# Performance work log

Measured on AMD Instinct MI355X. Metric: run time of the kernel, lower is better.

The kernel has to match this reference:

```python
import jax, jax.numpy as jnp
import numpy as np

B, T = 4, 2048
H, NH, NKV, HD = 2048, 16, 4, 128
THETA = 10000.0
SCALE = HD ** -0.5


def setup_inputs() -> dict:
    key = jax.random.key(0)
    ks = jax.random.split(key, 9)
    s = lambda n: 1.0 / np.sqrt(n)
    return {
        "hidden_states": jax.random.normal(ks[0], (B, T, H), jnp.float32),
        "positions": jnp.tile(jnp.arange(T, dtype=jnp.int32)[None, :], (B, 1)),
        "wq": jax.random.normal(ks[1], (H, NH * HD), jnp.float32) * s(H),
        "bq": jax.random.normal(ks[2], (NH * HD,), jnp.float32) * 0.01,
        "wk": jax.random.normal(ks[3], (H, NKV * HD), jnp.float32) * s(H),
        "bk": jax.random.normal(ks[4], (NKV * HD,), jnp.float32) * 0.01,
        "wv": jax.random.normal(ks[5], (H, NKV * HD), jnp.float32) * s(H),
        "bv": jax.random.normal(ks[6], (NKV * HD,), jnp.float32) * 0.01,
        "wo": jax.random.normal(ks[7], (NH * HD, H), jnp.float32) * s(NH * HD),
    }


def _rope(x, pos):
    # Neox-style RoPE over full head_dim. x: [B,T,n,HD], pos: [B,T]
    half = HD // 2
    inv_freq = 1.0 / (THETA ** (jnp.arange(half, dtype=jnp.float32) / half))
    freqs = pos.astype(jnp.float32)[..., None] * inv_freq  # [B,T,half]
    cos = jnp.cos(freqs)[:, :, None, :]
    sin = jnp.sin(freqs)[:, :, None, :]
    x1, x2 = x[..., :half], x[..., half:]
    return jnp.concatenate([x1 * cos - x2 * sin, x2 * cos + x1 * sin], axis=-1)


def reference(hidden_states, wq, bq, wk, bk, wv, bv, wo, positions):
    q = (hidden_states @ wq + bq).reshape(B, T, NH, HD)
    k = (hidden_states @ wk + bk).reshape(B, T, NKV, HD)
    v = (hidden_states @ wv + bv).reshape(B, T, NKV, HD)
    q = _rope(q, positions)
    k = _rope(k, positions)
    # GQA: repeat kv heads to match query heads
    rep = NH // NKV
    k = jnp.repeat(k, rep, axis=2)
    v = jnp.repeat(v, rep, axis=2)
    q = q.transpose(0, 2, 1, 3)  # [B,NH,T,HD]
    k = k.transpose(0, 2, 1, 3)
    v = v.transpose(0, 2, 1, 3)
    scores = jnp.einsum('bhqd,bhkd->bhqk', q, k) * SCALE
    causal = jnp.tril(jnp.ones((T, T), dtype=jnp.bool_))
    scores = jnp.where(causal[None, None, :, :], scores, -jnp.inf)
    w = jax.nn.softmax(scores, axis=-1).astype(v.dtype)
    o = jnp.einsum('bhqk,bhkd->bhqd', w, v)
    o = o.transpose(0, 2, 1, 3).reshape(B, T, NH * HD)
    return o @ wo
```

## Files before the change

kernel.cpp:

```cpp
#include <hip/hip_runtime.h>
#include <hip/hip_bf16.h>

#define TSEQ 2048
#define BATCH 4
#define NH 16
#define NKV 4
#define HD 128
#define NQKV 3072
#define SCALE_ 0.08838834764831845f

typedef __bf16 bf16x8 __attribute__((ext_vector_type(8)));
typedef float f32x4 __attribute__((ext_vector_type(4)));

__device__ __forceinline__ unsigned short f2bf(float f) {
    union { float f; unsigned u; } v; v.f = f;
    unsigned r = v.u + 0x7fffu + ((v.u >> 16) & 1u);
    return (unsigned short)(r >> 16);
}
__device__ __forceinline__ float bf2f(unsigned short b) {
    union { unsigned u; float f; } v; v.u = ((unsigned)b) << 16; return v.f;
}

__global__ __launch_bounds__(256) void xconv(const float* __restrict__ in,
                                             unsigned short* __restrict__ out) {
    const size_t i = (size_t)blockIdx.x * 256 + threadIdx.x;
    const float4 v = ((const float4*)in)[i];
    union { unsigned short u[4]; int2 p; } o;
    o.u[0] = f2bf(v.x); o.u[1] = f2bf(v.y); o.u[2] = f2bf(v.z); o.u[3] = f2bf(v.w);
    ((int2*)out)[i] = o.p;
}

__global__ __launch_bounds__(256) void wtrans_kernel(const float* __restrict__ in,
                                                     unsigned short* __restrict__ out,
                                                     int inN, int K) {
    __shared__ unsigned short l[64][65];
    const int n0 = blockIdx.x * 64, k0 = blockIdx.y * 64;
    const int tid = threadIdx.x;
    const int r = tid >> 2, c0 = (tid & 3) * 16;
#pragma unroll
    for (int i = 0; i < 16; i += 4) {
        float4 v = *(const float4*)&in[(size_t)(k0 + r) * inN + n0 + c0 + i];
        l[c0 + i + 0][r] = f2bf(v.x);
        l[c0 + i + 1][r] = f2bf(v.y);
        l[c0 + i + 2][r] = f2bf(v.z);
        l[c0 + i + 3][r] = f2bf(v.w);
    }
    __syncthreads();
    unsigned short tmp[16];
#pragma unroll
    for (int i = 0; i < 16; ++i) tmp[i] = l[r][c0 + i];
    *(int4*)&out[(size_t)(n0 + r) * K + k0 + c0] = *(int4*)&tmp[0];
    *(int4*)&out[(size_t)(n0 + r) * K + k0 + c0 + 8] = *(int4*)&tmp[8];
}

__global__ __launch_bounds__(256) void bias_concat(const float* __restrict__ bq,
                                                   const float* __restrict__ bk,
                                                   const float* __restrict__ bv,
                                                   float* __restrict__ out) {
    int i = blockIdx.x * 256 + threadIdx.x;
    out[i] = (i < 2048) ? bq[i] : ((i < 2560) ? bk[i - 2048] : bv[i - 2560]);
}

template <bool BIAS, bool OUTBF16>
__global__ __launch_bounds__(512) void gemm256(const unsigned short* __restrict__ A,
                                               const unsigned short* __restrict__ Bt,
                                               const float* __restrict__ bias,
                                               void* __restrict__ Cout,
                                               int M, int N, int K, int mtiles) {
    __shared__ unsigned short lA[2][256 * 64];
    __shared__ unsigned short lB[2][256 * 64];
    const int tid = threadIdx.x, lane = tid & 63, wid = tid >> 6;
    const int wr = wid >> 2, wc = wid & 3;
    const int g = lane >> 4, lr = lane & 15;
    const int nwg = gridDim.x;
    const int q = nwg >> 3;
    const int wg = (blockIdx.x & 7) * q + (blockIdx.x >> 3);
    const int bm = (wg % mtiles) * 256, bn = (wg / mtiles) * 256;

    f32x4 acc[8][4];
#pragma unroll
    for (int m = 0; m < 8; ++m)
#pragma unroll
        for (int n = 0; n < 4; ++n) acc[m][n] = f32x4{0.f, 0.f, 0.f, 0.f};

    auto stage = [&](int buf, int k0) {
#pragma unroll
        for (int c = 0; c < 4; ++c) {
            const int soff = (c * 512 + tid) * 16;
            const int row = soff >> 7;
            const int chunk = ((soff >> 4) & 7) ^ (row & 7);
            const unsigned lbase = (unsigned)(c * 512 + wid * 64) * 16;
            __builtin_amdgcn_global_load_lds(
                (const __attribute__((address_space(1))) unsigned int*)
                    (A + (size_t)(bm + row) * K + k0 + chunk * 8),
                (__attribute__((address_space(3))) unsigned int*)((char*)lA[buf] + lbase),
                16, 0, 0);
            __builtin_amdgcn_global_load_lds(
                (const __attribute__((address_space(1))) unsigned int*)
                    (Bt + (size_t)(bn + row) * K + k0 + chunk * 8),
                (__attribute__((address_space(3))) unsigned int*)((char*)lB[buf] + lbase),
                16, 0, 0);
        }
    };

    stage(0, 0);
    const int NT = K >> 6;
    for (int t = 0; t < NT; ++t) {
        const int buf = t & 1;
        if (t + 1 < NT) stage(buf ^ 1, (t + 1) << 6);
        __builtin_amdgcn_sched_barrier(0);
        if (t + 1 < NT) {
            asm volatile("s_waitcnt vmcnt(8)" ::: "memory");
        } else {
            asm volatile("s_waitcnt vmcnt(0)" ::: "memory");
        }
        __builtin_amdgcn_s_barrier();
        __builtin_amdgcn_sched_barrier(0);
        const char* pa = (const char*)lA[buf];
        const char* pb = (const char*)lB[buf];
#pragma unroll
        for (int kk = 0; kk < 2; ++kk) {
            bf16x8 bfr[4];
#pragma unroll
            for (int n = 0; n < 4; ++n) {
                const int row = wc * 64 + n * 16 + lr;
                bfr[n] = *(const bf16x8*)(pb + row * 128 + ((((kk << 2) + g) ^ (row & 7)) << 4));
            }
#pragma unroll
            for (int mh = 0; mh < 2; ++mh) {
                bf16x8 af[4];
#pragma unroll
                for (int m = 0; m < 4; ++m) {
                    const int row = wr * 128 + (mh * 4 + m) * 16 + lr;
                    af[m] = *(const bf16x8*)(pa + row * 128 + ((((kk << 2) + g) ^ (row & 7)) << 4));
                }
                __builtin_amdgcn_s_setprio(1);
#pragma unroll
                for (int m = 0; m < 4; ++m)
#pragma unroll
                    for (int n = 0; n < 4; ++n)
                        acc[mh * 4 + m][n] = __builtin_amdgcn_mfma_f32_16x16x32_bf16(
                            af[m], bfr[n], acc[mh * 4 + m][n], 0, 0, 0);
                __builtin_amdgcn_s_setprio(0);
            }
        }
        __builtin_amdgcn_sched_barrier(0);
        __builtin_amdgcn_s_barrier();
    }
#pragma unroll
    for (int m = 0; m < 8; ++m)
#pragma unroll
        for (int n = 0; n < 4; ++n) {
            const int col = bn + wc * 64 + n * 16 + lr;
            const float bv = BIAS ? bias[col] : 0.f;
#pragma unroll
            for (int ii = 0; ii < 4; ++ii) {
                const int r = bm + wr * 128 + m * 16 + g * 4 + ii;
                const float v = acc[m][n][ii] + bv;
                if (OUTBF16)
                    ((unsigned short*)Cout)[(size_t)r * N + col] = f2bf(v);
                else
                    ((float*)Cout)[(size_t)r * N + col] = v;
            }
        }
}

__global__ __launch_bounds__(256) void rope_kernel(unsigned short* __restrict__ QKV,
                                                   const int* __restrict__ positions) {
    const int tid = threadIdx.x;
    const int i = tid & 63;
    const int bt = blockIdx.x * 4 + (tid >> 6);
    const int head = blockIdx.y;
    unsigned short* base =
        QKV + (size_t)bt * NQKV + (head < NH ? head * HD : 2048 + (head - NH) * HD);
    const float pos = (float)positions[bt];
    const float invf = __expf(-(float)i * (9.21034037198e0f / 64.0f));
    const float f = pos * invf;
    const float sc = (head < NH) ? SCALE_ : 1.0f;
    const float c = cosf(f) * sc, s = sinf(f) * sc;
    const float x1 = bf2f(base[i]);
    const float x2 = bf2f(base[i + 64]);
    base[i] = f2bf(x1 * c - x2 * s);
    base[i + 64] = f2bf(x2 * c + x1 * s);
}

__global__ __launch_bounds__(256) void vtrans_kernel(const unsigned short* __restrict__ QKV,
                                                     unsigned short* __restrict__ Vt) {
    __shared__ unsigned short l[16][128];
    const int tid = threadIdx.x;
    const int t0 = blockIdx.x * 16, kvh = blockIdx.y, b = blockIdx.z;
#pragma unroll
    for (int i = 0; i < 8; ++i) {
        const int t = (tid >> 7) + i * 2, d = tid & 127;
        l[t][d] = QKV[(size_t)(b * TSEQ + t0 + t) * NQKV + 2560 + kvh * HD + d];
    }
    __syncthreads();
    const int d = tid >> 1, th = (tid & 1) * 8;
    unsigned short tmp[8];
#pragma unroll
    for (int i = 0; i < 8; ++i) tmp[i] = l[th + i][d];
    *(int4*)&Vt[((size_t)(b * NKV + kvh) * HD + d) * TSEQ + t0 + th] = *(int4*)tmp;
}

__global__ __launch_bounds__(512) void attn_kernel(const unsigned short* __restrict__ QKV,
                                                   const unsigned short* __restrict__ Vt,
                                                   unsigned short* __restrict__ O) {
    __shared__ unsigned short lK[2][64 * HD];
    __shared__ unsigned short lV[2][HD * 64];
    __shared__ unsigned short lP[128 * 64];
    const int tid = threadIdx.x, lane = tid & 63, w = tid >> 6;
    const int g = lane >> 4, lr = lane & 15;
    const int pair = blockIdx.x;
    const int h = blockIdx.y, b = blockIdx.z;
    const int kvh = h >> 2;

    const unsigned short* kgbase = QKV + (size_t)(b * TSEQ) * NQKV + 2048 + kvh * HD;
    const unsigned short* vgbase = Vt + (size_t)(b * NKV + kvh) * HD * TSEQ;

    auto stage = [&](int buf, int k0) {
#pragma unroll
        for (int c = 0; c < 2; ++c) {
            const int soff = (c * 512 + tid) * 16;
            {
                const int row = soff >> 8;
                const int off = soff ^ ((row & 7) << 4);
                __builtin_amdgcn_global_load_lds(
                    (const __attribute__((address_space(1))) unsigned int*)
                        ((const char*)(kgbase + (size_t)(k0 + row) * NQKV) + (off & 255)),
                    (__attribute__((address_space(3))) unsigned int*)
                        ((char*)lK[buf] + (c * 512 + w * 64) * 16),
                    16, 0, 0);
            }
            {
                const int row = soff >> 7;
                const int off = soff ^ ((row & 7) << 4);
                __builtin_amdgcn_global_load_lds(
                    (const __attribute__((address_space(1))) unsigned int*)
                        ((const char*)(vgbase + (size_t)row * TSEQ + (size_t)k0) + (off & 127)),
                    (__attribute__((address_space(3))) unsigned int*)
                        ((char*)lV[buf] + (c * 512 + w * 64) * 16),
                    16, 0, 0);
            }
        }
    };

    int cur = 0;
#pragma unroll 1
    for (int ph = 0; ph < 2; ++ph) {
        const int q0 = (ph == 0 ? (15 - pair) : pair) * 128;

        bf16x8 qf[4];
        {
            const unsigned short* qp =
                QKV + (size_t)(b * TSEQ + q0 + 16 * w + lr) * NQKV + h * HD;
#pragma unroll
            for (int kk = 0; kk < 4; ++kk) qf[kk] = *(const bf16x8*)(qp + kk * 32 + g * 8);
        }
        f32x4 oacc[8];
#pragma unroll
        for (int i = 0; i < 8; ++i) oacc[i] = f32x4{0.f, 0.f, 0.f, 0.f};
        float mrow[4] = {-1e30f, -1e30f, -1e30f, -1e30f};
        float lrow[4] = {0.f, 0.f, 0.f, 0.f};

        stage(cur, 0);
        __syncthreads();

        const int klast = q0 + 64;
        for (int k0 = 0; k0 <= klast; k0 += 64) {
            const bool more = (k0 < klast);
            if (more) stage(cur ^ 1, k0 + 64);

            const char* kb = (const char*)lK[cur];
            const char* vb = (const char*)lV[cur];

            f32x4 s[4];
#pragma unroll
            for (int j = 0; j < 4; ++j) s[j] = f32x4{0.f, 0.f, 0.f, 0.f};
#pragma unroll
            for (int kk = 0; kk < 4; ++kk) {
#pragma unroll
                for (int j = 0; j < 4; ++j) {
                    const int row = j * 16 + lr;
                    const int boff = (row * 256 + kk * 64 + g * 16) ^ ((row & 7) << 4);
                    bf16x8 kf = *(const bf16x8*)(kb + boff);
                    s[j] = __builtin_amdgcn_mfma_f32_16x16x32_bf16(qf[kk], kf, s[j], 0, 0, 0);
                }
            }
            if (k0 + 63 > q0 + 16 * w) {
#pragma unroll
                for (int j = 0; j < 4; ++j)
#pragma unroll
                    for (int ii = 0; ii < 4; ++ii) {
                        const int kglob = k0 + j * 16 + lr;
                        const int qglob = q0 + 16 * w + 4 * g + ii;
                        if (kglob > qglob) s[j][ii] = -1e30f;
                    }
            }
            float mnew[4];
#pragma unroll
            for (int ii = 0; ii < 4; ++ii)
                mnew[ii] = fmaxf(fmaxf(s[0][ii], s[1][ii]), fmaxf(s[2][ii], s[3][ii]));
#pragma unroll
            for (int d = 1; d < 16; d <<= 1)
#pragma unroll
                for (int ii = 0; ii < 4; ++ii)
                    mnew[ii] = fmaxf(mnew[ii], __shfl_xor(mnew[ii], d, 64));
            bool need = false;
#pragma unroll
            for (int ii = 0; ii < 4; ++ii) need = need || (mnew[ii] > mrow[ii] + 8.0f);
            if (__any(need)) {
#pragma unroll
                for (int ii = 0; ii < 4; ++ii) {
                    const float mN = fmaxf(mrow[ii], mnew[ii]);
                    const float resc = __expf(mrow[ii] - mN);
                    mrow[ii] = mN;
                    lrow[ii] *= resc;
#pragma unroll
                    for (int nf = 0; nf < 8; ++nf) oacc[nf][ii] *= resc;
                }
            }
#pragma unroll
            for (int j = 0; j < 4; ++j)
#pragma unroll
                for (int ii = 0; ii < 4; ++ii) {
                    const float p = __expf(s[j][ii] - mrow[ii]);
                    lrow[ii] += p;
                    const int prow = 16 * w + 4 * g + ii;
                    const int boff = (prow * 128 + (j * 16 + lr) * 2) ^ ((prow & 7) << 4);
                    *(unsigned short*)((char*)lP + boff) = f2bf(p);
                }
#pragma unroll
            for (int kk = 0; kk < 2; ++kk) {
                const int arow = 16 * w + lr;
                const int aoff = (arow * 128 + kk * 64 + g * 16) ^ ((arow & 7) << 4);
                bf16x8 pf = *(const bf16x8*)((const char*)lP + aoff);
#pragma unroll
                for (int nf = 0; nf < 8; ++nf) {
                    const int vrow = nf * 16 + lr;
                    const int voff = (vrow * 128 + kk * 64 + g * 16) ^ ((vrow & 7) << 4);
                    bf16x8 vf = *(const bf16x8*)(vb + voff);
                    oacc[nf] = __builtin_amdgcn_mfma_f32_16x16x32_bf16(pf, vf, oacc[nf], 0, 0, 0);
                }
            }
            __syncthreads();
            cur ^= 1;
        }
#pragma unroll
        for (int d = 1; d < 16; d <<= 1)
#pragma unroll
            for (int ii = 0; ii < 4; ++ii) lrow[ii] += __shfl_xor(lrow[ii], d, 64);
#pragma unroll
        for (int nf = 0; nf < 8; ++nf)
#pragma unroll
            for (int ii = 0; ii < 4; ++ii) {
                const int qrow = q0 + 16 * w + 4 * g + ii;
                const int col = h * HD + nf * 16 + lr;
                O[(size_t)(b * TSEQ + qrow) * (NH * HD) + col] = f2bf(oacc[nf][ii] / lrow[ii]);
            }
    }
}

extern "C" void kernel_launch(void* const* d_in, const int* in_sizes, int n_in,
                              void* d_out, int out_size, void* d_ws, size_t ws_size,
                              hipStream_t stream) {
    const float* hs = (const float*)d_in[0];
    const int* positions = (const int*)d_in[1];
    const float* wq = (const float*)d_in[2];
    const float* bq = (const float*)d_in[3];
    const float* wk = (const float*)d_in[4];
    const float* bk = (const float*)d_in[5];
    const float* wv = (const float*)d_in[6];
    const float* bv = (const float*)d_in[7];
    const float* wo = (const float*)d_in[8];
    float* out = (float*)d_out;

    const size_t SZ_XB = (size_t)8192 * 2048 * 2;
    const size_t SZ_WQKV = (size_t)3072 * 2048 * 2;
    const size_t SZ_WOT = (size_t)2048 * 2048 * 2;
    const size_t SZ_BIAS = 3072 * 4;
    const size_t SZ_QKV = (size_t)8192 * 3072 * 2;
    const size_t SZ_VT = (size_t)BATCH * NKV * HD * TSEQ * 2;
    const size_t SZ_OB = (size_t)8192 * 2048 * 2;

    char* ws = (char*)d_ws;
    unsigned short *Xb, *WqkvT, *WoT, *QKVb, *Vtb, *Ob;
    float* bqkv;
    const size_t need = SZ_XB + SZ_WQKV + SZ_WOT + SZ_BIAS + SZ_QKV + SZ_VT + SZ_OB + 2048;
    size_t off = 0;
    auto take = [&](size_t n) { char* p = ws + off; off += (n + 255) & ~(size_t)255; return p; };
    if (ws_size >= need) {
        Xb = (unsigned short*)take(SZ_XB);
        WqkvT = (unsigned short*)take(SZ_WQKV);
        Vtb = (unsigned short*)take(SZ_VT);
        WoT = (unsigned short*)take(SZ_WOT);
        bqkv = (float*)take(SZ_BIAS);
        QKVb = (unsigned short*)take(SZ_QKV);
        Ob = (unsigned short*)take(SZ_OB);
    } else {
        char* od = (char*)d_out;
        Xb = (unsigned short*)od;
        WqkvT = (unsigned short*)(od + SZ_XB);
        Vtb = (unsigned short*)(od + SZ_XB + SZ_WQKV);
        WoT = (unsigned short*)take(SZ_WOT);
        bqkv = (float*)take(SZ_BIAS);
        QKVb = (unsigned short*)take(SZ_QKV);
        Ob = (unsigned short*)take(SZ_OB);
    }

    xconv<<<16384, 256, 0, stream>>>(hs, Xb);
    wtrans_kernel<<<dim3(32, 32), 256, 0, stream>>>(wq, WqkvT, 2048, 2048);
    wtrans_kernel<<<dim3(8, 32), 256, 0, stream>>>(wk, WqkvT + (size_t)2048 * 2048, 512, 2048);
    wtrans_kernel<<<dim3(8, 32), 256, 0, stream>>>(wv, WqkvT + (size_t)2560 * 2048, 512, 2048);
    wtrans_kernel<<<dim3(32, 32), 256, 0, stream>>>(wo, WoT, 2048, 2048);
    bias_concat<<<12, 256, 0, stream>>>(bq, bk, bv, bqkv);
    gemm256<true, true><<<384, 512, 0, stream>>>(Xb, WqkvT, bqkv, QKVb, 8192, 3072, 2048, 32);
    rope_kernel<<<dim3(2048, 20), 256, 0, stream>>>(QKVb, positions);
    vtrans_kernel<<<dim3(128, 4, 4), 256, 0, stream>>>(QKVb, Vtb);
    attn_kernel<<<dim3(8, 16, 4), 512, 0, stream>>>(QKVb, Vtb, Ob);
    gemm256<false, false><<<256, 512, 0, stream>>>(Ob, WoT, nullptr, out, 8192, 2048, 2048, 32);
}
```

Before: 434.1 us.

## Split GEMM K-tile into two half-stages with interleaved prefetch and compute

Restructures the gemm256 LDS pipeline so each 64-wide K tile is stored as two 32-wide halves. Loads for the next tile's halves are issued one at a time between the two compute segments, with finer vmcnt waits and barriers. The aim is to overlap global-to-LDS transfers with MFMA work at a finer grain and to avoid stalling on the whole next tile. In exchange there is an extra barrier per iteration, and the swizzle changes to a 4-chunk XOR, which may raise LDS bank conflicts.

```diff
diff --git a/kernel.cpp b/kernel.cpp
--- a/kernel.cpp
+++ b/kernel.cpp
@@ -67,8 +67,8 @@
                                                const float* __restrict__ bias,
                                                void* __restrict__ Cout,
                                                int M, int N, int K, int mtiles) {
-    __shared__ unsigned short lA[2][256 * 64];
-    __shared__ unsigned short lB[2][256 * 64];
+    __shared__ unsigned short lA[2][2][256 * 32];
+    __shared__ unsigned short lB[2][2][256 * 32];
     const int tid = threadIdx.x, lane = tid & 63, wid = tid >> 6;
     const int wr = wid >> 2, wc = wid & 3;
     const int g = lane >> 4, lr = lane & 15;
@@ -83,69 +83,79 @@
 #pragma unroll
         for (int n = 0; n < 4; ++n) acc[m][n] = f32x4{0.f, 0.f, 0.f, 0.f};
 
-    auto stage = [&](int buf, int k0) {
-#pragma unroll
-        for (int c = 0; c < 4; ++c) {
+    auto stageA = [&](int buf, int kh, int kcol) {
+#pragma unroll
+        for (int c = 0; c < 2; ++c) {
             const int soff = (c * 512 + tid) * 16;
-            const int row = soff >> 7;
-            const int chunk = ((soff >> 4) & 7) ^ (row & 7);
-            const unsigned lbase = (unsigned)(c * 512 + wid * 64) * 16;
+            const int row = soff >> 6;
+            const int chunk = ((soff >> 4) & 3) ^ (row & 3);
             __builtin_amdgcn_global_load_lds(
                 (const __attribute__((address_space(1))) unsigned int*)
-                    (A + (size_t)(bm + row) * K + k0 + chunk * 8),
-                (__attribute__((address_space(3))) unsigned int*)((char*)lA[buf] + lbase),
+                    (A + (size_t)(bm + row) * K + kcol + kh * 32 + chunk * 8),
+                (__attribute__((address_space(3))) unsigned int*)
+                    ((char*)lA[buf][kh] + (c * 512 + wid * 64) * 16),
                 16, 0, 0);
+        }
+    };
+    auto stageB = [&](int buf, int kh, int kcol) {
+#pragma unroll
+        for (int c = 0; c < 2; ++c) {
+            const int soff = (c * 512 + tid) * 16;
+            const int row = soff >> 6;
+            const int chunk = ((soff >> 4) & 3) ^ (row & 3);
             __builtin_amdgcn_global_load_lds(
                 (const __attribute__((address_space(1))) unsigned int*)
-                    (Bt + (size_t)(bn + row) * K + k0 + chunk * 8),
-                (__attribute__((address_space(3))) unsigned int*)((char*)lB[buf] + lbase),
+                    (Bt + (size_t)(bn + row) * K + kcol + kh * 32 + chunk * 8),
+                (__attribute__((address_space(3))) unsigned int*)
+                    ((char*)lB[buf][kh] + (c * 512 + wid * 64) * 16),
                 16, 0, 0);
         }
     };
 
-    stage(0, 0);
+    auto compute_seg = [&](int buf, int kk) {
+        const char* pa = (const char*)lA[buf][kk];
+        const char* pb = (const char*)lB[buf][kk];
+        bf16x8 bfr[4];
+#pragma unroll
+        for (int n = 0; n < 4; ++n) {
+            const int row = wc * 64 + n * 16 + lr;
+            bfr[n] = *(const bf16x8*)(pb + row * 64 + ((g ^ (row & 3)) << 4));
+        }
+        __builtin_amdgcn_s_setprio(1);
+#pragma unroll
+        for (int m = 0; m < 8; ++m) {
+            const int row = wr * 128 + m * 16 + lr;
+            bf16x8 af = *(const bf16x8*)(pa + row * 64 + ((g ^ (row & 3)) << 4));
+#pragma unroll
+            for (int n = 0; n < 4; ++n)
+                acc[m][n] = __builtin_amdgcn_mfma_f32_16x16x32_bf16(af, bfr[n], acc[m][n], 0, 0, 0);
+        }
+        __builtin_amdgcn_s_setprio(0);
+    };
+
+    stageA(0, 0, 0);
+    stageB(0, 0, 0);
+    stageA(0, 1, 0);
+    stageB(0, 1, 0);
+
     const int NT = K >> 6;
     for (int t = 0; t < NT; ++t) {
         const int buf = t & 1;
-        if (t + 1 < NT) stage(buf ^ 1, (t + 1) << 6);
-        __builtin_amdgcn_sched_barrier(0);
-        if (t + 1 < NT) {
-            asm volatile("s_waitcnt vmcnt(8)" ::: "memory");
-        } else {
-            asm volatile("s_waitcnt vmcnt(0)" ::: "memory");
-        }
+        const bool more = (t + 1 < NT);
+        const int kn = (t + 1) << 6;
+        asm volatile("s_waitcnt vmcnt(4)" ::: "memory");
         __builtin_amdgcn_s_barrier();
         __builtin_amdgcn_sched_barrier(0);
-        const char* pa = (const char*)lA[buf];
-        const char* pb = (const char*)lB[buf];
-#pragma unroll
-        for (int kk = 0; kk < 2; ++kk) {
-            bf16x8 bfr[4];
-#pragma unroll
-            for (int n = 0; n < 4; ++n) {
-                const int row = wc * 64 + n * 16 + lr;
-                bfr[n] = *(const bf16x8*)(pb + row * 128 + ((((kk << 2) + g) ^ (row & 7)) << 4));
-            }
-#pragma unroll
-            for (int mh = 0; mh < 2; ++mh) {
-                bf16x8 af[4];
-#pragma unroll
-                for (int m = 0; m < 4; ++m) {
-                    const int row = wr * 128 + (mh * 4 + m) * 16 + lr;
-                    af[m] = *(const bf16x8*)(pa + row * 128 + ((((kk << 2) + g) ^ (row & 7)) << 4));
-                }
-                __builtin_amdgcn_s_setprio(1);
-#pragma unroll
-                for (int m = 0; m < 4; ++m)
-#pragma unroll
-                    for (int n = 0; n < 4; ++n)
-                        acc[mh * 4 + m][n] = __builtin_amdgcn_mfma_f32_16x16x32_bf16(
-                            af[m], bfr[n], acc[mh * 4 + m][n], 0, 0, 0);
-                __builtin_amdgcn_s_setprio(0);
-            }
-        }
+        if (more) { stageA(buf ^ 1, 0, kn); stageB(buf ^ 1, 0, kn); }
+        compute_seg(buf, 0);
+        if (more)
+            asm volatile("s_waitcnt vmcnt(4)" ::: "memory");
+        else
+            asm volatile("s_waitcnt vmcnt(0)" ::: "memory");
+        __builtin_amdgcn_s_barrier();
         __builtin_amdgcn_sched_barrier(0);
-        __builtin_amdgcn_s_barrier();
+        if (more) { stageA(buf ^ 1, 1, kn); stageB(buf ^ 1, 1, kn); }
+        compute_seg(buf, 1);
     }
 #pragma unroll
     for (int m = 0; m < 8; ++m)
```

New measurement: 489.3 us. 1.13x slower.
